# Optimization experiments

Hardware: AMD Instinct MI355X
Metric: run time of the kernel (lower is better)

## Reference

```python
import jax, jax.numpy as jnp
import numpy as np

N = 4_194_304   # samples per polarization
L = 513         # impulse response taps


def setup_inputs() -> dict:
    key = jax.random.key(0)
    k1, k2, k3, k4 = jax.random.split(key, 4)
    tx_real = jax.random.normal(k1, (2, N), dtype=jnp.float32)
    tx_imag = jax.random.normal(k2, (2, N), dtype=jnp.float32)
    h_real = jax.random.normal(k3, (L,), dtype=jnp.float32)
    h_imag = jax.random.normal(k4, (L,), dtype=jnp.float32)
    return {"tx_real": tx_real, "tx_imag": tx_imag, "h_real": h_real, "h_imag": h_imag}


def reference(tx_real, tx_imag, h_real, h_imag):
    # Dual-pol complex baseband signal [2, N]; same taps h [L] applied to each pol.
    tx = tx_real + 1j * tx_imag          # complex64 [2, N]
    h = h_real + 1j * h_imag             # complex64 [L]
    n_out = tx.shape[-1] + h.shape[0] - 1  # 'full' convolution length
    # FFT-based full convolution, both polarizations batched in one FFT call
    # (mathematically identical to overlap-save convolution in 'full' mode).
    X = jnp.fft.fft(tx, n=n_out, axis=-1)   # [2, n_out]
    H = jnp.fft.fft(h, n=n_out)             # [n_out]
    y = jnp.fft.ifft(X * H[None, :], axis=-1)  # [2, n_out] complex
    # Return real/imag stacked so the output is a real array: [2, n_out, 2]
    return jnp.stack([y.real, y.imag], axis=-1)
```

## Files before the change

kernel.cpp:

```cpp
#include <hip/hip_runtime.h>
#include <hip/hip_bf16.h>


#define NSAMP 4194304
#define LTAPS 513
#define NOUT  (NSAMP + LTAPS - 1)

#define BLK       512
#define WAVE_OUT  1024
#define BLOCK_OUT 8192
#define HALO      512
#define XELEMS    (BLOCK_OUT + HALO + 16)
#define NB        34
#define HROWS     592
#define GRID      256
#define NT        513
#define SITER     5

typedef __attribute__((ext_vector_type(8)))  short short8;
typedef __attribute__((ext_vector_type(4)))  short short4v;
typedef __attribute__((ext_vector_type(4)))  int   int4v;
typedef __attribute__((ext_vector_type(16))) float float16v;

__device__ __forceinline__ int xswz(int e) { return e ^ (((e >> 6) & 7) << 3); }
#define XSZ XELEMS

__device__ __forceinline__ short f2b(float f) {
    __bf16 b = (__bf16)f;
    return __builtin_bit_cast(short, b);
}

__global__ __launch_bounds__(BLK)
void build_h(const float* __restrict__ hr, const float* __restrict__ hi,
             short* __restrict__ hh) {
    int R = blockIdx.x * BLK + threadIdx.x;
    if (R < HROWS) {
        short8 vr, vi;
        #pragma unroll
        for (int j = 0; j < 8; ++j) {
            int idx = R - 24 - j;
            bool ok = (idx >= 0) && (idx < LTAPS);
            vr[j] = f2b(ok ? hr[idx] : 0.0f);
            vi[j] = f2b(ok ? hi[idx] : 0.0f);
        }
        *(short8*)(hh + (size_t)(0 * HROWS + R) * 8) = vr;
        *(short8*)(hh + (size_t)(1 * HROWS + R) * 8) = vi;
    }
}

#define MFMA32(A, B, C) __builtin_amdgcn_mfma_f32_32x32x16_bf16((A), (B), (C), 0, 0, 0)

__device__ __forceinline__ short8 bneg8(short8 v) {
    int4v t = __builtin_bit_cast(int4v, v);
    t ^= (int4v){(int)0x80008000, (int)0x80008000, (int)0x80008000, (int)0x80008000};
    return __builtin_bit_cast(short8, t);
}

__device__ __forceinline__ bool tile_edge(int t) { return (t == 0) || (t >= 511); }

__global__ __launch_bounds__(BLK, 2)
void fir_pipe(const float* __restrict__ txr_all, const float* __restrict__ txi_all,
              const short* __restrict__ hh, float2* __restrict__ out) {
    const int bid = blockIdx.x;
    const int tid = threadIdx.x;

    __shared__ __align__(16) short xs[2][4][XSZ];
    __shared__ __align__(16) short hl[2 * HROWS * 8];

    {
        const int4* src = (const int4*)hh;
        int4* dst = (int4*)hl;
        #pragma unroll
        for (int it = 0; it < 3; ++it) {
            int idx = tid + it * BLK;
            if (idx < 2 * HROWS) dst[idx] = src[idx];
        }
    }

    auto stage_tile = [&](int t, int buf) {
        const int N0 = t * BLOCK_OUT;
        short* xnb = &xs[buf][0][0];
        for (int p = 0; p < 2; ++p) {
            const float* __restrict__ xr_g = txr_all + (size_t)p * NSAMP;
            const float* __restrict__ xi_g = txi_all + (size_t)p * NSAMP;
            for (int it = 0; it < SITER; ++it) {
                int e = (tid + it * BLK) * 4;
                if (e < XELEMS) {
                    int g = N0 - HALO + e;
                    float r0, r1, r2, r3, i0, i1, i2, i3;
                    if (g >= 0 && g + 3 < NSAMP) {
                        float4 frv = *(const float4*)(xr_g + g);
                        float4 fiv = *(const float4*)(xi_g + g);
                        r0 = frv.x; r1 = frv.y; r2 = frv.z; r3 = frv.w;
                        i0 = fiv.x; i1 = fiv.y; i2 = fiv.z; i3 = fiv.w;
                    } else {
                        int gc0 = min(max(g + 0, 0), NSAMP - 1);
                        int gc1 = min(max(g + 1, 0), NSAMP - 1);
                        int gc2 = min(max(g + 2, 0), NSAMP - 1);
                        int gc3 = min(max(g + 3, 0), NSAMP - 1);
                        r0 = (g + 0 >= 0 && g + 0 < NSAMP) ? xr_g[gc0] : 0.0f;
                        r1 = (g + 1 >= 0 && g + 1 < NSAMP) ? xr_g[gc1] : 0.0f;
                        r2 = (g + 2 >= 0 && g + 2 < NSAMP) ? xr_g[gc2] : 0.0f;
                        r3 = (g + 3 >= 0 && g + 3 < NSAMP) ? xr_g[gc3] : 0.0f;
                        i0 = (g + 0 >= 0 && g + 0 < NSAMP) ? xi_g[gc0] : 0.0f;
                        i1 = (g + 1 >= 0 && g + 1 < NSAMP) ? xi_g[gc1] : 0.0f;
                        i2 = (g + 2 >= 0 && g + 2 < NSAMP) ? xi_g[gc2] : 0.0f;
                        i3 = (g + 3 >= 0 && g + 3 < NSAMP) ? xi_g[gc3] : 0.0f;
                    }
                    int ls = xswz(e);
                    short4v vr = { f2b(r0), f2b(r1), f2b(r2), f2b(r3) };
                    short4v vi = { f2b(i0), f2b(i1), f2b(i2), f2b(i3) };
                    *(short4v*)(xnb + (size_t)(2 * p + 0) * XSZ + ls) = vr;
                    *(short4v*)(xnb + (size_t)(2 * p + 1) * XSZ + ls) = vi;
                }
            }
        }
    };

    const int lane = tid & 63;
    const int wave = tid >> 6;
    const int cc   = lane & 31;
    const int half = lane >> 5;
    const short* hp0  = hl + (size_t)(cc - 8 * half + 8) * 8;
    const int   ebase = HALO + wave * WAVE_OUT + 32 * cc + 8 * half + 16;

    stage_tile(bid, 0);
    asm volatile("s_waitcnt lgkmcnt(0)" ::: "memory");
    __builtin_amdgcn_s_barrier();
    __builtin_amdgcn_sched_barrier(0);

    int cur = 0;
    for (int t = bid; t < NT; t += GRID) {
        const int  tn = t + GRID;
        const bool do_stage = (tn < NT) && !tile_edge(tn);
        const int  N0 = t * BLOCK_OUT;
        const int  nw = N0 + wave * WAVE_OUT;
        const bool did = (nw < NOUT);

        float16v zero = {0.f,0.f,0.f,0.f,0.f,0.f,0.f,0.f,0.f,0.f,0.f,0.f,0.f,0.f,0.f,0.f};
        float16v acc_re0 = zero, acc_im0 = zero, acc_re1 = zero, acc_im1 = zero;

        if (did) {
            const short* xb  = &xs[cur][0][0];
            short*       xnb = &xs[cur ^ 1][0][0];
            const int    sg  = tn * BLOCK_OUT - HALO;
            float4 sr[10], si[10];

            #pragma unroll
            for (int b = 0; b < NB; ++b) {
                if ((b & 1) == 0 && b < 20) {
                    if (do_stage) {
                        const int j  = b >> 1;
                        const int p  = (j >= SITER) ? 1 : 0;
                        const int it = j - p * SITER;
                        const int e  = (tid + it * BLK) * 4;
                        if (e < XELEMS) {
                            const float* xr_g = txr_all + (size_t)p * NSAMP + sg + e;
                            const float* xi_g = txi_all + (size_t)p * NSAMP + sg + e;
                            sr[j] = *(const float4*)xr_g;
                            si[j] = *(const float4*)xi_g;
                        }
                    }
                }
                if ((b & 1) == 0 && b >= 8 && b < 28) {
                    if (do_stage) {
                        const int j  = (b - 8) >> 1;
                        const int p  = (j >= SITER) ? 1 : 0;
                        const int it = j - p * SITER;
                        const int e  = (tid + it * BLK) * 4;
                        if (e < XELEMS) {
                            int ls = xswz(e);
                            float4 r = sr[j], i = si[j];
                            short4v vr = { f2b(r.x), f2b(r.y), f2b(r.z), f2b(r.w) };
                            short4v vi = { f2b(i.x), f2b(i.y), f2b(i.z), f2b(i.w) };
                            *(short4v*)(xnb + (size_t)(2 * p + 0) * XSZ + ls) = vr;
                            *(short4v*)(xnb + (size_t)(2 * p + 1) * XSZ + ls) = vi;
                        }
                    }
                }

                int ls = xswz(ebase - 16 * b);
                short8 fxr0 = *(const short8*)(xb + ls);
                short8 fxi0 = *(const short8*)(xb + XSZ + ls);
                short8 fxr1 = *(const short8*)(xb + 2 * XSZ + ls);
                short8 fxi1 = *(const short8*)(xb + 3 * XSZ + ls);
                const short* hp = hp0 + (size_t)(16 * b) * 8;
                short8 fhr = *(const short8*)(hp);
                short8 fhi = *(const short8*)(hp + (size_t)HROWS * 8);

                short8 fnhi = bneg8(fhi);
                acc_re0 = MFMA32(fxr0, fhr,  acc_re0);
                acc_im0 = MFMA32(fxi0, fhr,  acc_im0);
                acc_re1 = MFMA32(fxr1, fhr,  acc_re1);
                acc_im1 = MFMA32(fxi1, fhr,  acc_im1);
                acc_re0 = MFMA32(fxi0, fnhi, acc_re0);
                acc_im0 = MFMA32(fxr0, fhi,  acc_im0);
                acc_re1 = MFMA32(fxi1, fnhi, acc_re1);
                acc_im1 = MFMA32(fxr1, fhi,  acc_im1);
            }
        }

        if (tn < NT && tile_edge(tn)) stage_tile(tn, cur ^ 1);

        asm volatile("s_waitcnt lgkmcnt(0)" ::: "memory");
        __builtin_amdgcn_s_barrier();
        __builtin_amdgcn_sched_barrier(0);

        if (did) {
            float2* __restrict__ op0 = out;
            float2* __restrict__ op1 = out + (size_t)NOUT;
            #pragma unroll
            for (int v = 0; v < 16; ++v) {
                int row = (v & 3) + 8 * (v >> 2) + 4 * half;
                int n = nw + 32 * row + cc;
                if (n < NOUT) {
                    op0[n] = make_float2(acc_re0[v], acc_im0[v]);
                    op1[n] = make_float2(acc_re1[v], acc_im1[v]);
                }
            }
        }
        cur ^= 1;
    }
}

extern "C" void kernel_launch(void* const* d_in, const int* in_sizes, int n_in,
                              void* d_out, int out_size, void* d_ws, size_t ws_size,
                              hipStream_t stream) {
    const float* txr = (const float*)d_in[0];
    const float* txi = (const float*)d_in[1];
    const float* hr  = (const float*)d_in[2];
    const float* hi  = (const float*)d_in[3];
    float2* out = (float2*)d_out;
    short* hh = (short*)d_ws;

    build_h<<<dim3((HROWS + BLK - 1) / BLK), BLK, 0, stream>>>(hr, hi, hh);

    fir_pipe<<<dim3(GRID), BLK, 0, stream>>>(txr, txi, hh, out);
}
```

Before: 139.3 us.

## Split FIR blocks into producer wave and consumer waves with LDS flag handshake

Restructures the FIR kernel into warp specialization: one wave per block loads input tiles from global memory, converts them to bf16 and writes them into double-buffered LDS, while three consumer waves run the MFMA convolution. They synchronize through LDS ready and done counters with spin-waits instead of block-wide barriers. Tiles shrink to 3072 outputs, blocks to 256 threads, and the grid grows to 512 blocks. The aim is to decouple load latency from MFMA work, at the cost of spin-wait overhead, a single producer wave whose bandwidth may limit throughput, and possible ordering hazards in the handshake.

Result: slower. 152.8 us (+9.6%).

```diff
diff --git a/kernel.cpp b/kernel.cpp
--- a/kernel.cpp
+++ b/kernel.cpp
@@ -6,16 +6,16 @@
 #define LTAPS 513
 #define NOUT  (NSAMP + LTAPS - 1)
 
-#define BLK       512
-#define WAVE_OUT  1024
-#define BLOCK_OUT 8192
+#define BLK       256
+#define NCONS     3
+#define TILE_OUT  3072
 #define HALO      512
-#define XELEMS    (BLOCK_OUT + HALO + 16)
+#define XELEMS    (TILE_OUT + HALO + 16)
 #define NB        34
 #define HROWS     592
-#define GRID      256
-#define NT        513
-#define SITER     5
+#define GRID      512
+#define NT        ((NOUT + TILE_OUT - 1) / TILE_OUT)
+#define CITERS    15
 
 typedef __attribute__((ext_vector_type(8)))  short short8;
 typedef __attribute__((ext_vector_type(4)))  short short4v;
@@ -56,170 +56,183 @@
     return __builtin_bit_cast(short8, t);
 }
 
-__device__ __forceinline__ bool tile_edge(int t) { return (t == 0) || (t >= 511); }
-
 __global__ __launch_bounds__(BLK, 2)
-void fir_pipe(const float* __restrict__ txr_all, const float* __restrict__ txi_all,
-              const short* __restrict__ hh, float2* __restrict__ out) {
-    const int bid = blockIdx.x;
-    const int tid = threadIdx.x;
+void fir_pc(const float* __restrict__ txr_all, const float* __restrict__ txi_all,
+            const short* __restrict__ hh, float2* __restrict__ out) {
+    const int bid  = blockIdx.x;
+    const int tid  = threadIdx.x;
+    const int lane = tid & 63;
+    const int wave = tid >> 6;
 
     __shared__ __align__(16) short xs[2][4][XSZ];
     __shared__ __align__(16) short hl[2 * HROWS * 8];
-
-    {
-        const int4* src = (const int4*)hh;
-        int4* dst = (int4*)hl;
-        #pragma unroll
-        for (int it = 0; it < 3; ++it) {
-            int idx = tid + it * BLK;
-            if (idx < 2 * HROWS) dst[idx] = src[idx];
-        }
-    }
-
-    auto stage_tile = [&](int t, int buf) {
-        const int N0 = t * BLOCK_OUT;
-        short* xnb = &xs[buf][0][0];
-        for (int p = 0; p < 2; ++p) {
-            const float* __restrict__ xr_g = txr_all + (size_t)p * NSAMP;
-            const float* __restrict__ xi_g = txi_all + (size_t)p * NSAMP;
-            for (int it = 0; it < SITER; ++it) {
-                int e = (tid + it * BLK) * 4;
-                if (e < XELEMS) {
-                    int g = N0 - HALO + e;
-                    float r0, r1, r2, r3, i0, i1, i2, i3;
-                    if (g >= 0 && g + 3 < NSAMP) {
-                        float4 frv = *(const float4*)(xr_g + g);
-                        float4 fiv = *(const float4*)(xi_g + g);
-                        r0 = frv.x; r1 = frv.y; r2 = frv.z; r3 = frv.w;
-                        i0 = fiv.x; i1 = fiv.y; i2 = fiv.z; i3 = fiv.w;
-                    } else {
-                        int gc0 = min(max(g + 0, 0), NSAMP - 1);
-                        int gc1 = min(max(g + 1, 0), NSAMP - 1);
-                        int gc2 = min(max(g + 2, 0), NSAMP - 1);
-                        int gc3 = min(max(g + 3, 0), NSAMP - 1);
-                        r0 = (g + 0 >= 0 && g + 0 < NSAMP) ? xr_g[gc0] : 0.0f;
-                        r1 = (g + 1 >= 0 && g + 1 < NSAMP) ? xr_g[gc1] : 0.0f;
-                        r2 = (g + 2 >= 0 && g + 2 < NSAMP) ? xr_g[gc2] : 0.0f;
-                        r3 = (g + 3 >= 0 && g + 3 < NSAMP) ? xr_g[gc3] : 0.0f;
-                        i0 = (g + 0 >= 0 && g + 0 < NSAMP) ? xi_g[gc0] : 0.0f;
-                        i1 = (g + 1 >= 0 && g + 1 < NSAMP) ? xi_g[gc1] : 0.0f;
-                        i2 = (g + 2 >= 0 && g + 2 < NSAMP) ? xi_g[gc2] : 0.0f;
-                        i3 = (g + 3 >= 0 && g + 3 < NSAMP) ? xi_g[gc3] : 0.0f;
-                    }
-                    int ls = xswz(e);
-                    short4v vr = { f2b(r0), f2b(r1), f2b(r2), f2b(r3) };
-                    short4v vi = { f2b(i0), f2b(i1), f2b(i2), f2b(i3) };
-                    *(short4v*)(xnb + (size_t)(2 * p + 0) * XSZ + ls) = vr;
-                    *(short4v*)(xnb + (size_t)(2 * p + 1) * XSZ + ls) = vi;
+    __shared__ int rdy[2];
+    __shared__ int done[2];
+
+    if (tid < 2) { rdy[tid] = 0; done[tid] = 0; }
+    __syncthreads();
+
+    const int pwave = (bid & 1) ? 3 : 0;
+
+    if (wave == pwave) {
+        {
+            const int4* src = (const int4*)hh;
+            int4* dst = (int4*)hl;
+            #pragma unroll
+            for (int it = 0; it < 19; ++it) {
+                int idx = lane + it * 64;
+                if (idx < 2 * HROWS) dst[idx] = src[idx];
+            }
+        }
+
+        for (int t = bid, g = 0; t < NT; t += GRID, ++g) {
+            const int buf = g & 1;
+            if (g >= 2) {
+                const int need = NCONS * (g >> 1);
+                while (__hip_atomic_load(&done[buf], __ATOMIC_ACQUIRE,
+                                         __HIP_MEMORY_SCOPE_WORKGROUP) < need)
+                    __builtin_amdgcn_s_sleep(1);
+            }
+
+            if (t != 0 && t != NT - 1) {
+                const long gb = (long)t * TILE_OUT - HALO;
+                const float* cp0 = txr_all + gb;
+                const float* cp1 = txi_all + gb;
+                const float* cp2 = txr_all + (size_t)NSAMP + gb;
+                const float* cp3 = txi_all + (size_t)NSAMP + gb;
+                const float* cps[4] = { cp0, cp1, cp2, cp3 };
+                float4 vb[2][CITERS];
+
+                #define PLOAD(c)                                               \
+                    _Pragma("unroll")                                          \
+                    for (int j = 0; j < CITERS; ++j) {                         \
+                        int e = (lane + 64 * j) * 4;                           \
+                        if (e < XELEMS)                                        \
+                            vb[(c) & 1][j] = *(const float4*)(cps[(c)] + e);   \
+                    }
+                #define PWRITE(c)                                              \
+                    _Pragma("unroll")                                          \
+                    for (int j = 0; j < CITERS; ++j) {                         \
+                        int e = (lane + 64 * j) * 4;                           \
+                        if (e < XELEMS) {                                      \
+                            float4 v = vb[(c) & 1][j];                         \
+                            short4v s = { f2b(v.x), f2b(v.y),                  \
+                                          f2b(v.z), f2b(v.w) };                \
+                            *(short4v*)(&xs[buf][(c)][xswz(e)]) = s;           \
+                        }                                                      \
+                    }
+                PLOAD(0);
+                __builtin_amdgcn_sched_barrier(0);
+                PLOAD(1);
+                __builtin_amdgcn_sched_barrier(0);
+                PWRITE(0);
+                __builtin_amdgcn_sched_barrier(0);
+                PLOAD(2);
+                __builtin_amdgcn_sched_barrier(0);
+                PWRITE(1);
+                __builtin_amdgcn_sched_barrier(0);
+                PLOAD(3);
+                __builtin_amdgcn_sched_barrier(0);
+                PWRITE(2);
+                __builtin_amdgcn_sched_barrier(0);
+                PWRITE(3);
+                #undef PLOAD
+                #undef PWRITE
+            } else {
+                const int N0 = t * TILE_OUT;
+                for (int c = 0; c < 4; ++c) {
+                    const int p = c >> 1;
+                    const float* xg = ((c & 1) ? txi_all : txr_all) + (size_t)p * NSAMP;
+                    for (int j = 0; j < CITERS; ++j) {
+                        int e = (lane + 64 * j) * 4;
+                        if (e < XELEMS) {
+                            int g0 = N0 - HALO + e;
+                            float v0, v1, v2, v3;
+                            if (g0 >= 0 && g0 + 3 < NSAMP) {
+                                float4 fv = *(const float4*)(xg + g0);
+                                v0 = fv.x; v1 = fv.y; v2 = fv.z; v3 = fv.w;
+                            } else {
+                                int c0 = min(max(g0 + 0, 0), NSAMP - 1);
+                                int c1 = min(max(g0 + 1, 0), NSAMP - 1);
+                                int c2 = min(max(g0 + 2, 0), NSAMP - 1);
+                                int c3 = min(max(g0 + 3, 0), NSAMP - 1);
+                                v0 = (g0 + 0 >= 0 && g0 + 0 < NSAMP) ? xg[c0] : 0.0f;
+                                v1 = (g0 + 1 >= 0 && g0 + 1 < NSAMP) ? xg[c1] : 0.0f;
+                                v2 = (g0 + 2 >= 0 && g0 + 2 < NSAMP) ? xg[c2] : 0.0f;
+                                v3 = (g0 + 3 >= 0 && g0 + 3 < NSAMP) ? xg[c3] : 0.0f;
+                            }
+                            short4v s = { f2b(v0), f2b(v1), f2b(v2), f2b(v3) };
+                            *(short4v*)(&xs[buf][c][xswz(e)]) = s;
+                        }
+                    }
                 }
             }
-        }
-    };
-
-    const int lane = tid & 63;
-    const int wave = tid >> 6;
-    const int cc   = lane & 31;
-    const int half = lane >> 5;
-    const short* hp0  = hl + (size_t)(cc - 8 * half + 8) * 8;
-    const int   ebase = HALO + wave * WAVE_OUT + 32 * cc + 8 * half + 16;
-
-    stage_tile(bid, 0);
-    asm volatile("s_waitcnt lgkmcnt(0)" ::: "memory");
-    __builtin_amdgcn_s_barrier();
-    __builtin_amdgcn_sched_barrier(0);
-
-    int cur = 0;
-    for (int t = bid; t < NT; t += GRID) {
-        const int  tn = t + GRID;
-        const bool do_stage = (tn < NT) && !tile_edge(tn);
-        const int  N0 = t * BLOCK_OUT;
-        const int  nw = N0 + wave * WAVE_OUT;
-        const bool did = (nw < NOUT);
-
-        float16v zero = {0.f,0.f,0.f,0.f,0.f,0.f,0.f,0.f,0.f,0.f,0.f,0.f,0.f,0.f,0.f,0.f};
-        float16v acc_re0 = zero, acc_im0 = zero, acc_re1 = zero, acc_im1 = zero;
-
-        if (did) {
-            const short* xb  = &xs[cur][0][0];
-            short*       xnb = &xs[cur ^ 1][0][0];
-            const int    sg  = tn * BLOCK_OUT - HALO;
-            float4 sr[10], si[10];
-
-            #pragma unroll
-            for (int b = 0; b < NB; ++b) {
-                if ((b & 1) == 0 && b < 20) {
-                    if (do_stage) {
-                        const int j  = b >> 1;
-                        const int p  = (j >= SITER) ? 1 : 0;
-                        const int it = j - p * SITER;
-                        const int e  = (tid + it * BLK) * 4;
-                        if (e < XELEMS) {
-                            const float* xr_g = txr_all + (size_t)p * NSAMP + sg + e;
-                            const float* xi_g = txi_all + (size_t)p * NSAMP + sg + e;
-                            sr[j] = *(const float4*)xr_g;
-                            si[j] = *(const float4*)xi_g;
-                        }
-                    }
+
+            asm volatile("s_waitcnt lgkmcnt(0)" ::: "memory");
+            if (lane == 0)
+                __hip_atomic_store(&rdy[buf], g + 1, __ATOMIC_RELEASE,
+                                   __HIP_MEMORY_SCOPE_WORKGROUP);
+        }
+    } else {
+        const int ci   = (wave < pwave) ? wave : wave - 1;
+        const int cc   = lane & 31;
+        const int half = lane >> 5;
+        const short* hp0  = hl + (size_t)(cc - 8 * half + 8) * 8;
+        const int   ebase = HALO + ci * 1024 + 32 * cc + 8 * half + 16;
+
+        for (int t = bid, g = 0; t < NT; t += GRID, ++g) {
+            const int buf = g & 1;
+            while (__hip_atomic_load(&rdy[buf], __ATOMIC_ACQUIRE,
+                                     __HIP_MEMORY_SCOPE_WORKGROUP) < g + 1)
+                __builtin_amdgcn_s_sleep(1);
+
+            const int nw = t * TILE_OUT + ci * 1024;
+            if (nw < NOUT) {
+                float16v zero = {0.f,0.f,0.f,0.f,0.f,0.f,0.f,0.f,
+                                 0.f,0.f,0.f,0.f,0.f,0.f,0.f,0.f};
+                float16v acc_re0 = zero, acc_im0 = zero;
+                float16v acc_re1 = zero, acc_im1 = zero;
+                const short* xb = &xs[buf][0][0];
+
+                #pragma unroll
+                for (int b = 0; b < NB; ++b) {
+                    int ls = xswz(ebase - 16 * b);
+                    short8 fxr0 = *(const short8*)(xb + ls);
+                    short8 fxi0 = *(const short8*)(xb + XSZ + ls);
+                    short8 fxr1 = *(const short8*)(xb + 2 * XSZ + ls);
+                    short8 fxi1 = *(const short8*)(xb + 3 * XSZ + ls);
+                    const short* hp = hp0 + (size_t)(16 * b) * 8;
+                    short8 fhr = *(const short8*)(hp);
+                    short8 fhi = *(const short8*)(hp + (size_t)HROWS * 8);
+
+                    short8 fnhi = bneg8(fhi);
+                    acc_re0 = MFMA32(fxr0, fhr,  acc_re0);
+                    acc_im0 = MFMA32(fxi0, fhr,  acc_im0);
+                    acc_re1 = MFMA32(fxr1, fhr,  acc_re1);
+                    acc_im1 = MFMA32(fxi1, fhr,  acc_im1);
+                    acc_re0 = MFMA32(fxi0, fnhi, acc_re0);
+                    acc_im0 = MFMA32(fxr0, fhi,  acc_im0);
+                    acc_re1 = MFMA32(fxi1, fnhi, acc_re1);
+                    acc_im1 = MFMA32(fxr1, fhi,  acc_im1);
                 }
-                if ((b & 1) == 0 && b >= 8 && b < 28) {
-                    if (do_stage) {
-                        const int j  = (b - 8) >> 1;
-                        const int p  = (j >= SITER) ? 1 : 0;
-                        const int it = j - p * SITER;
-                        const int e  = (tid + it * BLK) * 4;
-                        if (e < XELEMS) {
-                            int ls = xswz(e);
-                            float4 r = sr[j], i = si[j];
-                            short4v vr = { f2b(r.x), f2b(r.y), f2b(r.z), f2b(r.w) };
-                            short4v vi = { f2b(i.x), f2b(i.y), f2b(i.z), f2b(i.w) };
-                            *(short4v*)(xnb + (size_t)(2 * p + 0) * XSZ + ls) = vr;
-                            *(short4v*)(xnb + (size_t)(2 * p + 1) * XSZ + ls) = vi;
-                        }
+
+                float2* __restrict__ op0 = out;
+                float2* __restrict__ op1 = out + (size_t)NOUT;
+                #pragma unroll
+                for (int v = 0; v < 16; ++v) {
+                    int row = (v & 3) + 8 * (v >> 2) + 4 * half;
+                    int n = nw + 32 * row + cc;
+                    if (n < NOUT) {
+                        op0[n] = make_float2(acc_re0[v], acc_im0[v]);
+                        op1[n] = make_float2(acc_re1[v], acc_im1[v]);
                     }
                 }
-
-                int ls = xswz(ebase - 16 * b);
-                short8 fxr0 = *(const short8*)(xb + ls);
-                short8 fxi0 = *(const short8*)(xb + XSZ + ls);
-                short8 fxr1 = *(const short8*)(xb + 2 * XSZ + ls);
-                short8 fxi1 = *(const short8*)(xb + 3 * XSZ + ls);
-                const short* hp = hp0 + (size_t)(16 * b) * 8;
-                short8 fhr = *(const short8*)(hp);
-                short8 fhi = *(const short8*)(hp + (size_t)HROWS * 8);
-
-                short8 fnhi = bneg8(fhi);
-                acc_re0 = MFMA32(fxr0, fhr,  acc_re0);
-                acc_im0 = MFMA32(fxi0, fhr,  acc_im0);
-                acc_re1 = MFMA32(fxr1, fhr,  acc_re1);
-                acc_im1 = MFMA32(fxi1, fhr,  acc_im1);
-                acc_re0 = MFMA32(fxi0, fnhi, acc_re0);
-                acc_im0 = MFMA32(fxr0, fhi,  acc_im0);
-                acc_re1 = MFMA32(fxi1, fnhi, acc_re1);
-                acc_im1 = MFMA32(fxr1, fhi,  acc_im1);
-            }
-        }
-
-        if (tn < NT && tile_edge(tn)) stage_tile(tn, cur ^ 1);
-
-        asm volatile("s_waitcnt lgkmcnt(0)" ::: "memory");
-        __builtin_amdgcn_s_barrier();
-        __builtin_amdgcn_sched_barrier(0);
-
-        if (did) {
-            float2* __restrict__ op0 = out;
-            float2* __restrict__ op1 = out + (size_t)NOUT;
-            #pragma unroll
-            for (int v = 0; v < 16; ++v) {
-                int row = (v & 3) + 8 * (v >> 2) + 4 * half;
-                int n = nw + 32 * row + cc;
-                if (n < NOUT) {
-                    op0[n] = make_float2(acc_re0[v], acc_im0[v]);
-                    op1[n] = make_float2(acc_re1[v], acc_im1[v]);
-                }
-            }
-        }
-        cur ^= 1;
+            }
+
+            if (lane == 0)
+                __hip_atomic_fetch_add(&done[buf], 1, __ATOMIC_RELEASE,
+                                       __HIP_MEMORY_SCOPE_WORKGROUP);
+        }
     }
 }
 
@@ -235,5 +248,5 @@
 
     build_h<<<dim3((HROWS + BLK - 1) / BLK), BLK, 0, stream>>>(hr, hi, hh);
 
-    fir_pipe<<<dim3(GRID), BLK, 0, stream>>>(txr, txi, hh, out);
-}
+    fir_pc<<<dim3(GRID), BLK, 0, stream>>>(txr, txi, hh, out);
+}
```
